# Kernel optimization log

Hardware: AMD Instinct MI355X
Metric: run time of the kernel (lower is better)

The kernel has to match this reference:

```python
import jax, jax.numpy as jnp
import numpy as np

B, S, HID = 2, 2048, 2048
H, KV, D = 16, 4, 128
G = H // KV  # kv groups
THETA = 10000.0


def setup_inputs() -> dict:
    key = jax.random.key(0)
    ks = jax.random.split(key, 6)
    x = jax.random.normal(ks[0], (B, S, HID), dtype=jnp.float32)
    wq = jax.random.normal(ks[1], (HID, H * D), dtype=jnp.float32) * 0.02
    wk = jax.random.normal(ks[2], (HID, KV * D), dtype=jnp.float32) * 0.02
    wv = jax.random.normal(ks[3], (HID, KV * D), dtype=jnp.float32) * 0.02
    wo = jax.random.normal(ks[4], (H * D, HID), dtype=jnp.float32) * 0.02
    # RoPE freqs: complex exp(i * pos * theta^{-2j/D}) -> cos/sin of shape [S, D//2]
    inv_freq = 1.0 / (THETA ** (jnp.arange(0, D, 2, dtype=jnp.float32) / D))
    ang = jnp.arange(S, dtype=jnp.float32)[:, None] * inv_freq[None, :]
    return {"x": x, "freqs_cos": jnp.cos(ang), "freqs_sin": jnp.sin(ang),
            "wq": wq, "wk": wk, "wv": wv, "wo": wo}


def _apply_rope(t, cos, sin):
    # t: [B, h, S, D]; cos/sin: [S, D//2]; complex multiply on interleaved pairs
    tr = t.reshape(*t.shape[:-1], -1, 2)
    x1, x2 = tr[..., 0], tr[..., 1]
    c = cos[None, None, :, :]
    s = sin[None, None, :, :]
    out = jnp.stack([x1 * c - x2 * s, x1 * s + x2 * c], axis=-1)
    return out.reshape(t.shape)


def reference(x, freqs_cos, freqs_sin, wq, wk, wv, wo):
    b, s, _ = x.shape
    q = (x @ wq).reshape(b, s, H, D).transpose(0, 2, 1, 3)   # [B,H,S,D]
    k = (x @ wk).reshape(b, s, KV, D).transpose(0, 2, 1, 3)  # [B,KV,S,D]
    v = (x @ wv).reshape(b, s, KV, D).transpose(0, 2, 1, 3)
    q = _apply_rope(q, freqs_cos, freqs_sin)
    k = _apply_rope(k, freqs_cos, freqs_sin)
    # GQA: group Q heads per KV head instead of expanding K/V
    qg = q.reshape(b, KV, G, s, D)
    scale = 1.0 / jnp.sqrt(jnp.asarray(D, dtype=x.dtype))
    scores = jnp.einsum('bkgqd,bksd->bkgqs', qg, k) * scale  # [B,KV,G,S,S]
    causal = jnp.tril(jnp.ones((s, s), dtype=bool))
    scores = jnp.where(causal[None, None, None], scores, jnp.finfo(scores.dtype).min)
    attn = jax.nn.softmax(scores, axis=-1)
    out = jnp.einsum('bkgqs,bksd->bkgqd', attn, v)           # [B,KV,G,S,D]
    out = out.reshape(b, H, s, D).transpose(0, 2, 1, 3).reshape(b, s, H * D)
    return (out @ wo, k, v)
```

## Files before the change

### kernel.cpp

```cpp
#include <hip/hip_runtime.h>
#include <stdint.h>

#define BB 2
#define SS 2048
#define HIDD 2048
#define HH 16
#define KVH 4
#define DD 128
#define KDIM 2048

typedef short bf16x4 __attribute__((ext_vector_type(4)));
typedef short bf16x8 __attribute__((ext_vector_type(8)));
typedef float f32x4 __attribute__((ext_vector_type(4)));
typedef float f32x16 __attribute__((ext_vector_type(16)));

__device__ __forceinline__ unsigned short f2b(float f) {
  union { float f; unsigned u; } v; v.f = f;
  unsigned r = v.u + 0x7FFFu + ((v.u >> 16) & 1u);
  return (unsigned short)(r >> 16);
}

__device__ __forceinline__ float b2f(unsigned short u) {
  union { unsigned u; float f; } v; v.u = ((unsigned)u) << 16;
  return v.f;
}

__device__ __forceinline__ unsigned cvtpk_bf16(float a, float b) {
  unsigned r;
  asm("v_cvt_pk_bf16_f32 %0, %1, %2" : "=v"(r) : "v"(a), "v"(b));
  return r;
}

__device__ __forceinline__ void gload16(const unsigned short* g, unsigned short* l) {
  __builtin_amdgcn_global_load_lds(
      (const __attribute__((address_space(1))) unsigned int*)(g),
      (__attribute__((address_space(3))) unsigned int*)(l), 16, 0, 0);
}

__device__ __forceinline__ bf16x8 ldT(const char* lds, int byteoff) {
  union { bf16x8 v; int4 q; } u;
  u.q = *reinterpret_cast<const int4*>(lds + byteoff);
  return u.v;
}

template <int N>
__device__ __forceinline__ void waitv() {
  if constexpr (N == 0) asm volatile("s_waitcnt vmcnt(0)" ::: "memory");
  else if constexpr (N == 1) asm volatile("s_waitcnt vmcnt(1)" ::: "memory");
  else if constexpr (N == 2) asm volatile("s_waitcnt vmcnt(2)" ::: "memory");
  else if constexpr (N == 3) asm volatile("s_waitcnt vmcnt(3)" ::: "memory");
  else if constexpr (N == 4) asm volatile("s_waitcnt vmcnt(4)" ::: "memory");
  else asm volatile("s_waitcnt vmcnt(6)" ::: "memory");
}

__global__ __launch_bounds__(256) void k_convert(const float* __restrict__ in,
                                                 unsigned short* __restrict__ out, int n4) {
  int i = blockIdx.x * 256 + threadIdx.x;
  int stride = gridDim.x * 256;
  for (; i < n4; i += stride) {
    float4 v = reinterpret_cast<const float4*>(in)[i];
    ushort4 o;
    o.x = f2b(v.x); o.y = f2b(v.y); o.z = f2b(v.z); o.w = f2b(v.w);
    int ci = i & 511;
    int t = ci & 7;
    int ci2 = (ci & ~7) | ((t & 3) << 1) | (t >> 2);
    reinterpret_cast<ushort4*>(out)[(i & ~511) | ci2] = o;
  }
}

__global__ __launch_bounds__(256) void k_transpose(const float* __restrict__ in,
                                                   unsigned short* __restrict__ out,
                                                   int K, int N) {
  __shared__ float tile[32][33];
  int n0 = blockIdx.x * 32, k0 = blockIdx.y * 32;
  int tx = threadIdx.x, ty = threadIdx.y;
#pragma unroll
  for (int j = 0; j < 32; j += 8)
    tile[ty + j][tx] = in[(size_t)(k0 + ty + j) * N + n0 + tx];
  __syncthreads();
  int kp = ((tx >> 2) & 3) * 8 + (tx & 3) + ((tx >> 4) << 2);
#pragma unroll
  for (int j = 0; j < 32; j += 8)
    out[(size_t)(n0 + ty + j) * K + k0 + kp] = f2b(tile[tx][ty + j]);
}

template <int EPI, int BM>
__global__ __launch_bounds__(512) void k_gemm8(
    const unsigned short* __restrict__ A, const unsigned short* __restrict__ Bt,
    float* __restrict__ outF, unsigned short* __restrict__ qws,
    unsigned short* __restrict__ kws, unsigned short* __restrict__ vTws,
    float* __restrict__ koutF, float* __restrict__ voutF,
    const float* __restrict__ cosT, const float* __restrict__ sinT) {
  constexpr int LA = BM / 128;
  constexpr int LB = 2;
  constexpr int ASTR = BM * 64;
  constexpr int BSTR = 256 * 64;
  constexpr int MF = BM / 64;
  constexpr int LSH = (BM == 256) ? 6 : 5;
  extern __shared__ __align__(16) unsigned short smem[];
  unsigned short* lAb = smem;
  unsigned short* lBb = smem + 2 * ASTR;

  const int bid = blockIdx.y * gridDim.x + blockIdx.x;
  const int nwg = gridDim.x * gridDim.y;
  const int mt = gridDim.x;
  const int swz = (bid & 7) * (nwg >> 3) + (bid >> 3);
  const int rowbase = (swz % mt) * BM;
  const int colbase = (swz / mt) * 256;

  const int tid = threadIdx.x;
  const int wv = tid >> 6, lane = tid & 63;
  const int wr = wv >> 2, wc = wv & 3;
  const int g = lane >> 4, c = lane & 15;

  const int srow8 = lane >> 3;
  const int gch = (lane & 7) ^ srow8;
  const unsigned short* aS[LA][2];
  const unsigned short* bS[2][2];
  int aOff[LA][2], bOff[2][2];
#pragma unroll
  for (int j = 0; j < LA; ++j)
#pragma unroll
    for (int h = 0; h < 2; ++h) {
      int s = wv * LA + j;
      int q = s * 8 + srow8;
      int rA = (q >> LSH) * (BM / 2) + h * (BM / 4) + (q & (BM / 4 - 1));
      aS[j][h] = A + (size_t)(rowbase + rA) * KDIM + gch * 8;
      aOff[j][h] = (h * (BM / 2) + s * 8) * 64;
    }
#pragma unroll
  for (int j = 0; j < 2; ++j)
#pragma unroll
    for (int h = 0; h < 2; ++h) {
      int s = wv * 2 + j;
      int q = s * 8 + srow8;
      int rB = (q >> 5) * 64 + h * 32 + (q & 31);
      bS[j][h] = Bt + (size_t)(colbase + rB) * KDIM + gch * 8;
      bOff[j][h] = (h * 128 + s * 8) * 64;
    }

  f32x4 acc[2 * MF][4] = {};
  bf16x8 af[MF][2], bfr[4][2];
  const int NT = KDIM / 64;

#define STAGE_A(buf, kt, h)                                               \
  _Pragma("unroll") for (int j = 0; j < LA; ++j)                          \
      gload16(aS[j][h] + (kt) * 64, lAb + (buf) * ASTR + aOff[j][h]);
#define STAGE_B(buf, kt, h)                                               \
  _Pragma("unroll") for (int j = 0; j < 2; ++j)                           \
      gload16(bS[j][h] + (kt) * 64, lBb + (buf) * BSTR + bOff[j][h]);
#define LDA(buf, mh)                                                      \
  _Pragma("unroll") for (int mm = 0; mm < MF; ++mm) {                     \
    int sr = (mh) * (BM / 2) + wr * (BM / 4) + mm * 16 + c;               \
    _Pragma("unroll") for (int kk = 0; kk < 2; ++kk) {                    \
      int slot = (kk * 4 + g) ^ (c & 7);                                  \
      af[mm][kk] = *reinterpret_cast<const bf16x8*>(                      \
          lAb + (buf) * ASTR + sr * 64 + slot * 8);                       \
    } }
#define LDB(buf, nh)                                                      \
  _Pragma("unroll") for (int nn = 0; nn < 2; ++nn) {                      \
    int sr = (nh) * 128 + wc * 32 + nn * 16 + c;                          \
    _Pragma("unroll") for (int kk = 0; kk < 2; ++kk) {                    \
      int slot = (kk * 4 + g) ^ (c & 7);                                  \
      bfr[(nh) * 2 + nn][kk] = *reinterpret_cast<const bf16x8*>(          \
          lBb + (buf) * BSTR + sr * 64 + slot * 8);                       \
    } }
#define MM(mh, nh)                                                        \
  _Pragma("unroll") for (int mm = 0; mm < MF; ++mm)                       \
  _Pragma("unroll") for (int nn = 0; nn < 2; ++nn)                        \
  _Pragma("unroll") for (int kk = 0; kk < 2; ++kk)                        \
    acc[(mh) * MF + mm][(nh) * 2 + nn] =                                  \
        __builtin_amdgcn_mfma_f32_16x16x32_bf16(                          \
            af[mm][kk], bfr[(nh) * 2 + nn][kk],                           \
            acc[(mh) * MF + mm][(nh) * 2 + nn], 0, 0, 0);
#define SCHB __builtin_amdgcn_sched_barrier(0);
#define SB __builtin_amdgcn_s_barrier();
#define LGKM asm volatile("s_waitcnt lgkmcnt(0)" ::: "memory");
#define MFMAWIN(mh, nh)                                                   \
  LGKM SCHB __builtin_amdgcn_s_setprio(1);                                \
  MM(mh, nh) __builtin_amdgcn_s_setprio(0); SCHB SB

  STAGE_A(0, 0, 0) STAGE_B(0, 0, 0) STAGE_B(0, 0, 1) STAGE_A(0, 0, 1)
  waitv<LA + LB>(); SCHB SB

  for (int kt = 0; kt < NT - 1; ++kt) {
    const int buf = kt & 1, nbuf = buf ^ 1;
    LDA(buf, 0) LDB(buf, 0)
    STAGE_A(nbuf, kt + 1, 0)
    waitv<2 * LA>(); SCHB SB
    MFMAWIN(0, 0)
    LDB(buf, 1)
    STAGE_B(nbuf, kt + 1, 0)
    waitv<LA + LB>(); SCHB SB
    MFMAWIN(0, 1)
    LDA(buf, 1)
    STAGE_B(nbuf, kt + 1, 1)
    SCHB SB
    MFMAWIN(1, 0)
    STAGE_A(nbuf, kt + 1, 1)
    waitv<LA + LB>(); SCHB SB
    MFMAWIN(1, 1)
  }
  {
    const int buf = (NT - 1) & 1;
    LDA(buf, 0) LDB(buf, 0)
    waitv<LA>(); SCHB SB
    MFMAWIN(0, 0)
    LDB(buf, 1)
    waitv<0>(); SCHB SB
    MFMAWIN(0, 1)
    LDA(buf, 1)
    SCHB SB
    MFMAWIN(1, 0)
    __builtin_amdgcn_s_setprio(1);
    MM(1, 1)
    __builtin_amdgcn_s_setprio(0);
  }

  if (EPI == 0) {
#pragma unroll
    for (int m = 0; m < 2 * MF; ++m)
#pragma unroll
      for (int n = 0; n < 4; ++n)
#pragma unroll
        for (int i = 0; i < 4; ++i) {
          int R = rowbase + wr * (BM / 2) + m * 16 + g * 4 + i;
          int Cc = colbase + wc * 64 + n * 16 + c;
          outF[(size_t)R * 2048 + Cc] = acc[m][n][i];
        }
  } else {
#pragma unroll
    for (int m = 0; m < 2 * MF; ++m) {
#pragma unroll
      for (int n = 0; n < 4; ++n) {
#pragma unroll
        for (int i = 0; i < 4; ++i) {
          float val = acc[m][n][i];
          float partner = __shfl_xor(val, 1, 64);
          int R = rowbase + wr * (BM / 2) + m * 16 + g * 4 + i;
          int Cc = colbase + wc * 64 + n * 16 + c;
          int b = R >> 11, s = R & 2047;
          int d = Cc & 127;
          int j = d >> 1;
          float cs = cosT[s * 64 + j], sn = sinT[s * 64 + j];
          float ro = ((d & 1) == 0) ? (val * cs - partner * sn)
                                    : (partner * sn + val * cs);
          if (Cc < 2048) {
            int h = Cc >> 7;
            qws[((size_t)(b * HH + h) * SS + s) * DD + d] = f2b(ro);
          } else if (Cc < 2560) {
            int kvh = (Cc - 2048) >> 7;
            size_t idx = ((size_t)(b * KVH + kvh) * SS + s) * DD + d;
            koutF[idx] = ro;
            int d16 = d & 15;
            int dp = (d & ~15) | (d16 & 3) | ((d16 & 4) << 1) | ((d16 & 8) >> 1);
            kws[((size_t)(b * KVH + kvh) * SS + s) * DD + dp] = f2b(ro);
          } else {
            int kvh = (Cc - 2560) >> 7;
            size_t idx = ((size_t)(b * KVH + kvh) * SS + s) * DD + d;
            voutF[idx] = val;
            int s16 = s & 15;
            int sp = (s & ~15) | (s16 & 3) | ((s16 & 4) << 1) | ((s16 & 8) >> 1);
            vTws[((size_t)(b * KVH + kvh) * DD + d) * SS + sp] = f2b(val);
          }
        }
      }
    }
  }
#undef STAGE_A
#undef STAGE_B
#undef LDA
#undef LDB
#undef MM
#undef SCHB
#undef SB
#undef LGKM
#undef MFMAWIN
}

__constant__ int JC[24] = {7,15,15,14,14,6,13,13,12,12,5,11,11,10,10,4,9,9,8,8,3,2,1,0};
__constant__ int JP[24] = {0,0,1, 0,1, 0,0,1, 0,1, 0,0,1, 0,1, 0,0,1, 0,1, 0,0,0,0};

__global__ __launch_bounds__(256, 2) void k_attn(const unsigned short* __restrict__ qws,
                                                 const unsigned short* __restrict__ kws,
                                                 const unsigned short* __restrict__ vT,
                                                 unsigned short* __restrict__ aows,
                                                 unsigned short* __restrict__ pO,
                                                 float* __restrict__ pml) {
  __shared__ __align__(16) char lds[2][32768];
  const int tid = threadIdx.x;
  const int lane = tid & 63;
  const int w = tid >> 6;
  const int lq = lane & 31;
  const int hi = lane >> 5;

  const int bid = blockIdx.x;
  const int j = bid >> 5;
  const int y = bid & 31;
  const int head = 4 * (y & 7) + ((y >> 3) & 3);
  const int c = JC[j];
  const int part = JP[j];
  const bool split = (c >= 8);
  const int tstart = split ? (part ? (c + 1) : 0) : 0;
  const int tend = split ? (part ? (2 * c + 2) : (c + 1)) : (2 * c + 2);

  const int b = head >> 4, h = head & 15;
  const int kv = h >> 2;
  const int q0w = c * 128 + w * 32;
  const int qg = q0w + lq;
  const float cl2 = 0.12751743f;

  const unsigned short* qp = qws + ((size_t)(b * HH + h) * SS + qg) * DD;
  bf16x8 qf[8];
#pragma unroll
  for (int ks = 0; ks < 8; ++ks) {
    union { bf16x8 v8; bf16x4 v4[2]; } u;
    const unsigned short* p = qp + ks * 16 + hi * 4;
    u.v4[0] = *reinterpret_cast<const bf16x4*>(p);
    u.v4[1] = *reinterpret_cast<const bf16x4*>(p + 8);
    qf[ks] = u.v8;
  }

  const unsigned short* kbase = kws + (size_t)(b * KVH + kv) * SS * DD;
  const unsigned short* vbase = vT + (size_t)(b * KVH + kv) * DD * SS;

  const unsigned short* kSrc[4];
  const unsigned short* vSrc[4];
  int ldsOff[4];
#pragma unroll
  for (int j2 = 0; j2 < 4; ++j2) {
    int i = w + 4 * j2;
    int ks = i >> 1, half = i & 1;
    kSrc[j2] = kbase + (size_t)(half * 32 + (lane >> 1)) * DD + ks * 16 + (lane & 1) * 8;
    int kkv = i >> 2, d0v = i & 3;
    vSrc[j2] = vbase + (size_t)(d0v * 32 + (lane >> 1)) * SS + kkv * 16 + (lane & 1) * 8;
    ldsOff[j2] = i * 1024;
  }

  auto STAGE = [&](int t, int buf) {
    char* lK = lds[buf];
    char* lV = lds[buf] + 16384;
#pragma unroll
    for (int j2 = 0; j2 < 4; ++j2) {
      gload16(kSrc[j2] + (size_t)t * 64 * DD, (unsigned short*)(lK + ldsOff[j2]));
      gload16(vSrc[j2] + (size_t)t * 64, (unsigned short*)(lV + ldsOff[j2]));
    }
  };

  f32x16 o[4] = {};
  float mrow = -1e30f, lrow = 0.f;

  STAGE(tstart, 0);
  STAGE(tstart + 1, 1);
  asm volatile("s_waitcnt vmcnt(8)" ::: "memory");
  __builtin_amdgcn_sched_barrier(0);
  __builtin_amdgcn_s_barrier();

  for (int t = tstart; t < tend; ++t) {
    const int cur = (t - tstart) & 1;

    if (t * 64 <= q0w + 31) {
      const char* lK = lds[cur];
      const char* lV = lds[cur] + 16384;
      const bool full2 = (t * 64 + 32 <= q0w + 31);

      f32x16 s0 = {}, s1 = {};
      __builtin_amdgcn_s_setprio(1);
#pragma unroll
      for (int ks = 0; ks < 8; ++ks) {
        int off = ks * 2048 + lq * 32 + hi * 16;
        s0 = __builtin_amdgcn_mfma_f32_32x32x16_bf16(ldT(lK, off), qf[ks], s0, 0, 0, 0);
      }
      if (full2) {
#pragma unroll
        for (int ks = 0; ks < 8; ++ks) {
          int off = ks * 2048 + 1024 + lq * 32 + hi * 16;
          s1 = __builtin_amdgcn_mfma_f32_32x32x16_bf16(ldT(lK, off), qf[ks], s1, 0, 0, 0);
        }
      }
      __builtin_amdgcn_s_setprio(0);

      const int kq = t * 64 + 4 * hi - qg;
      float p[32];
      float rowmax = -1e30f;
      const bool m0 = (t * 64 + 31) > q0w;
#pragma unroll
      for (int r = 0; r < 16; ++r) {
        float v = s0[r] * cl2;
        if (m0) {
          int kl = (r & 3) + 8 * (r >> 2);
          if (kq + kl > 0) v = -1e30f;
        }
        p[r] = v;
        rowmax = fmaxf(rowmax, v);
      }
      if (full2) {
        const bool m1 = (t * 64 + 63) > q0w;
#pragma unroll
        for (int r = 0; r < 16; ++r) {
          float v = s1[r] * cl2;
          if (m1) {
            int kl = 32 + (r & 3) + 8 * (r >> 2);
            if (kq + kl > 0) v = -1e30f;
          }
          p[16 + r] = v;
          rowmax = fmaxf(rowmax, v);
        }
      }
      rowmax = fmaxf(rowmax, __shfl_xor(rowmax, 32, 64));

      if (__any(rowmax > mrow + 8.f)) {
        float mnew = fmaxf(mrow, rowmax);
        float fac = exp2f(mrow - mnew);
        mrow = mnew;
        lrow *= fac;
#pragma unroll
        for (int d0 = 0; d0 < 4; ++d0)
#pragma unroll
          for (int r = 0; r < 16; ++r) o[d0][r] *= fac;
      }

      float rsum = 0.f;
#pragma unroll
      for (int e = 0; e < 16; ++e) { p[e] = exp2f(p[e] - mrow); rsum += p[e]; }
      if (full2) {
#pragma unroll
        for (int e = 16; e < 32; ++e) { p[e] = exp2f(p[e] - mrow); rsum += p[e]; }
      }
      rsum += __shfl_xor(rsum, 32, 64);
      lrow += rsum;

      bf16x8 pf[4];
#pragma unroll
      for (int s4 = 0; s4 < 2; ++s4) {
        union { bf16x8 v; unsigned u[4]; } pu;
        int base = s4 * 8;
#pragma unroll
        for (int jj = 0; jj < 4; ++jj)
          pu.u[jj] = cvtpk_bf16(p[base + 2 * jj], p[base + 2 * jj + 1]);
        pf[s4] = pu.v;
      }
      if (full2) {
#pragma unroll
        for (int s4 = 2; s4 < 4; ++s4) {
          union { bf16x8 v; unsigned u[4]; } pu;
          int base = 16 + (s4 - 2) * 8;
#pragma unroll
          for (int jj = 0; jj < 4; ++jj)
            pu.u[jj] = cvtpk_bf16(p[base + 2 * jj], p[base + 2 * jj + 1]);
          pf[s4] = pu.v;
        }
      }

      __builtin_amdgcn_s_setprio(1);
#pragma unroll
      for (int d0 = 0; d0 < 4; ++d0)
#pragma unroll
        for (int kk = 0; kk < 2; ++kk) {
          int off = (kk * 4 + d0) * 1024 + lq * 32 + hi * 16;
          o[d0] = __builtin_amdgcn_mfma_f32_32x32x16_bf16(ldT(lV, off), pf[kk], o[d0], 0, 0, 0);
        }
      if (full2) {
#pragma unroll
        for (int d0 = 0; d0 < 4; ++d0)
#pragma unroll
          for (int kk = 2; kk < 4; ++kk) {
            int off = (kk * 4 + d0) * 1024 + lq * 32 + hi * 16;
            o[d0] = __builtin_amdgcn_mfma_f32_32x32x16_bf16(ldT(lV, off), pf[kk], o[d0], 0, 0, 0);
          }
      }
      __builtin_amdgcn_s_setprio(0);
    }

    if (t + 1 < tend) {
      __builtin_amdgcn_s_barrier();
      if (t + 2 < tend) {
        STAGE(t + 2, cur);
        asm volatile("s_waitcnt vmcnt(8)" ::: "memory");
      } else {
        asm volatile("s_waitcnt vmcnt(0)" ::: "memory");
      }
      __builtin_amdgcn_sched_barrier(0);
      __builtin_amdgcn_s_barrier();
    }
  }

  if (!split) {
    float linv = 1.f / lrow;
    unsigned short* op = aows + ((size_t)(b * SS + qg)) * 2048 + h * 128;
#pragma unroll
    for (int d0 = 0; d0 < 4; ++d0)
#pragma unroll
      for (int rq = 0; rq < 4; ++rq) {
        unsigned w0 = cvtpk_bf16(o[d0][rq * 4 + 0] * linv, o[d0][rq * 4 + 1] * linv);
        unsigned w1 = cvtpk_bf16(o[d0][rq * 4 + 2] * linv, o[d0][rq * 4 + 3] * linv);
        int2 st2; st2.x = (int)w0; st2.y = (int)w1;
        int pos = 8 * ((2 * rq + hi) & 3) + 4 * (rq >> 1);
        *reinterpret_cast<int2*>(op + d0 * 32 + pos) = st2;
      }
  } else {
    int c8 = c - 8;
    int row = qg - c * 128;
    unsigned short* op = pO + ((((size_t)(head * 8 + c8) * 2 + part) * 128) + row) * 128;
#pragma unroll
    for (int d0 = 0; d0 < 4; ++d0)
#pragma unroll
      for (int rq = 0; rq < 4; ++rq) {
        unsigned w0 = cvtpk_bf16(o[d0][rq * 4 + 0], o[d0][rq * 4 + 1]);
        unsigned w1 = cvtpk_bf16(o[d0][rq * 4 + 2], o[d0][rq * 4 + 3]);
        int2 st2; st2.x = (int)w0; st2.y = (int)w1;
        *reinterpret_cast<int2*>(op + d0 * 32 + rq * 8 + hi * 4) = st2;
      }
    if (hi == 0) {
      int mlbase = (((head * 8 + c8) * 2 + part) * 2) * 128 + row;
      pml[mlbase] = mrow;
      pml[mlbase + 128] = lrow;
    }
  }
}

__global__ __launch_bounds__(256) void k_combine(const unsigned short* __restrict__ pO,
                                                 const float* __restrict__ pml,
                                                 unsigned short* __restrict__ aows) {
  int tid = blockIdx.x * 256 + threadIdx.x;
  int rg = tid >> 4;
  int d8 = tid & 15;
  int head = rg >> 10;
  int rem = rg & 1023;
  int c8 = rem >> 7;
  int row = rem & 127;
  int base2 = (head * 8 + c8) * 2;

  float m1 = pml[((base2 + 0) * 2 + 0) * 128 + row];
  float l1 = pml[((base2 + 0) * 2 + 1) * 128 + row];
  float m2 = pml[((base2 + 1) * 2 + 0) * 128 + row];
  float l2 = pml[((base2 + 1) * 2 + 1) * 128 + row];
  float m = fmaxf(m1, m2);
  float w1 = exp2f(m1 - m), w2 = exp2f(m2 - m);
  float inv = 1.f / (w1 * l1 + w2 * l2);

  const unsigned short* o1 = pO + (((size_t)(base2 + 0) * 128 + row) * 128) + d8 * 8;
  const unsigned short* o2 = pO + (((size_t)(base2 + 1) * 128 + row) * 128) + d8 * 8;
  union { int4 q; unsigned short us[8]; } ua, ub;
  ua.q = *reinterpret_cast<const int4*>(o1);
  ub.q = *reinterpret_cast<const int4*>(o2);
  float out[8];
#pragma unroll
  for (int e = 0; e < 8; ++e)
    out[e] = (w1 * b2f(ua.us[e]) + w2 * b2f(ub.us[e])) * inv;

  int b = head >> 4, h = head & 15;
  int s = (c8 + 8) * 128 + row;
  unsigned short* dst = aows + ((size_t)(b * SS + s)) * 2048 + h * 128;
  int d = d8 * 8;
  int dbase = d & ~31;
#pragma unroll
  for (int jj = 0; jj < 2; ++jj) {
    int t = ((d >> 2) + jj) & 7;
    int pos = ((t & 3) << 3) + ((t >> 2) << 2);
    unsigned wa = cvtpk_bf16(out[jj * 4 + 0], out[jj * 4 + 1]);
    unsigned wb = cvtpk_bf16(out[jj * 4 + 2], out[jj * 4 + 3]);
    int2 st2; st2.x = (int)wa; st2.y = (int)wb;
    *reinterpret_cast<int2*>(dst + dbase + pos) = st2;
  }
}

extern "C" void kernel_launch(void* const* d_in, const int* in_sizes, int n_in,
                              void* d_out, int out_size, void* d_ws, size_t ws_size,
                              hipStream_t stream) {
  (void)in_sizes; (void)n_in; (void)out_size; (void)ws_size;
  const float* x  = (const float*)d_in[0];
  const float* fc = (const float*)d_in[1];
  const float* fs = (const float*)d_in[2];
  const float* wq = (const float*)d_in[3];
  const float* wk = (const float*)d_in[4];
  const float* wv = (const float*)d_in[5];
  const float* wo = (const float*)d_in[6];
  float* out = (float*)d_out;
  float* koutF = out + (size_t)BB * SS * HIDD;
  float* voutF = koutF + (size_t)BB * KVH * SS * DD;

  unsigned short* wcatT = (unsigned short*)d_ws;
  unsigned short* woT   = wcatT + (size_t)3072 * 2048;
  unsigned short* xbf   = woT + (size_t)2048 * 2048;
  unsigned short* qws   = xbf + (size_t)4096 * 2048;
  unsigned short* kws   = qws + (size_t)BB * HH * SS * DD;
  unsigned short* vTws  = kws + (size_t)BB * KVH * SS * DD;
  unsigned short* aows  = vTws + (size_t)BB * KVH * DD * SS;

  unsigned short* pO = xbf;
  float* pml = (float*)wcatT;

  hipFuncSetAttribute((const void*)k_gemm8<1, 256>,
                      hipFuncAttributeMaxDynamicSharedMemorySize, 131072);
  hipFuncSetAttribute((const void*)k_gemm8<0, 128>,
                      hipFuncAttributeMaxDynamicSharedMemorySize, 98304);

  k_convert<<<2048, 256, 0, stream>>>(x, xbf, (int)((size_t)4096 * 2048 / 4));
  dim3 tb(32, 8);
  k_transpose<<<dim3(64, 64), tb, 0, stream>>>(wq, wcatT, 2048, 2048);
  k_transpose<<<dim3(16, 64), tb, 0, stream>>>(wk, wcatT + (size_t)2048 * 2048, 2048, 512);
  k_transpose<<<dim3(16, 64), tb, 0, stream>>>(wv, wcatT + (size_t)2560 * 2048, 2048, 512);
  k_transpose<<<dim3(64, 64), tb, 0, stream>>>(wo, woT, 2048, 2048);

  k_gemm8<1, 256><<<dim3(16, 12), 512, 131072, stream>>>(xbf, wcatT, nullptr, qws, kws,
                                                         vTws, koutF, voutF, fc, fs);
  k_attn<<<768, 256, 0, stream>>>(qws, kws, vTws, aows, pO, pml);
  k_combine<<<2048, 256, 0, stream>>>(pO, pml, aows);
  k_gemm8<0, 128><<<dim3(32, 8), 512, 98304, stream>>>(aows, woT, out, nullptr, nullptr,
                                                       nullptr, nullptr, nullptr, nullptr, nullptr);
}
```

Before: 235.8 us.

## Replace QKV projection GEMM with 128x192-tile kernel for more workgroups

Adds a dedicated QKV projection GEMM using 128x192 output tiles with a simple double-buffered direct-to-LDS pipeline, launching 512 workgroups instead of 192. The aim is better CU occupancy on a 256-CU device, where the 256x256 tiling left many CUs idle. The old fused RoPE/scatter epilogue moves into the new kernel, and the old templated GEMM is reduced to the plain output-projection path. The trade-offs are a simpler pipeline without the hand-tuned MFMA interleaving and more redundant loads of A and B tiles.

```diff
diff --git a/kernel.cpp b/kernel.cpp
--- a/kernel.cpp
+++ b/kernel.cpp
@@ -50,8 +50,10 @@
   else if constexpr (N == 2) asm volatile("s_waitcnt vmcnt(2)" ::: "memory");
   else if constexpr (N == 3) asm volatile("s_waitcnt vmcnt(3)" ::: "memory");
   else if constexpr (N == 4) asm volatile("s_waitcnt vmcnt(4)" ::: "memory");
+  else if constexpr (N == 5) asm volatile("s_waitcnt vmcnt(5)" ::: "memory");
   else asm volatile("s_waitcnt vmcnt(6)" ::: "memory");
 }
+
 
 __global__ __launch_bounds__(256) void k_convert(const float* __restrict__ in,
                                                  unsigned short* __restrict__ out, int n4) {
@@ -84,12 +86,136 @@
     out[(size_t)(n0 + ty + j) * K + k0 + kp] = f2b(tile[tx][ty + j]);
 }
 
+__global__ __launch_bounds__(512, 4) void k_gemm12(
+    const unsigned short* __restrict__ A, const unsigned short* __restrict__ Bt,
+    unsigned short* __restrict__ qws, unsigned short* __restrict__ kws,
+    unsigned short* __restrict__ vTws, float* __restrict__ koutF,
+    float* __restrict__ voutF, const float* __restrict__ cosT,
+    const float* __restrict__ sinT) {
+  __shared__ __align__(16) unsigned short lA[2][128 * 64];
+  __shared__ __align__(16) unsigned short lB[2][192 * 64];
+  const int bid = blockIdx.y * gridDim.x + blockIdx.x;
+  const int swz = (bid & 7) * 64 + (bid >> 3);
+  const int rowbase = (swz & 31) * 128;
+  const int colbase = (swz >> 5) * 192;
+  const int tid = threadIdx.x;
+  const int wv = tid >> 6, lane = tid & 63;
+  const int wr = wv >> 2, wc = wv & 3;
+  const int g = lane >> 4, c = lane & 15;
+
+  const unsigned short* aSrc[2];
+  const unsigned short* bSrc[3];
+  int aDst[2], bDst[3];
+#pragma unroll
+  for (int j = 0; j < 2; ++j) {
+    int idx = j * 512 + tid;
+    int row = idx >> 3, sl = idx & 7;
+    int gch = sl ^ (row & 7);
+    aSrc[j] = A + (size_t)(rowbase + row) * KDIM + gch * 8;
+    aDst[j] = idx * 8;
+  }
+#pragma unroll
+  for (int j = 0; j < 3; ++j) {
+    int idx = j * 512 + tid;
+    int row = idx >> 3, sl = idx & 7;
+    int gch = sl ^ (row & 7);
+    bSrc[j] = Bt + (size_t)(colbase + row) * KDIM + gch * 8;
+    bDst[j] = idx * 8;
+  }
+
+  f32x4 acc[4][3] = {};
+  const int NT = KDIM / 64;
+
+  auto STAGE = [&](int buf, int kt) {
+#pragma unroll
+    for (int j = 0; j < 2; ++j)
+      gload16(aSrc[j] + kt * 64, &lA[buf][0] + aDst[j]);
+#pragma unroll
+    for (int j = 0; j < 3; ++j)
+      gload16(bSrc[j] + kt * 64, &lB[buf][0] + bDst[j]);
+  };
+
+  STAGE(0, 0);
+  STAGE(1, 1);
+
+  for (int t = 0; t < NT; ++t) {
+    if (t + 1 < NT) { waitv<5>(); } else { waitv<0>(); }
+    __builtin_amdgcn_sched_barrier(0);
+    __builtin_amdgcn_s_barrier();
+
+    const unsigned short* la = lA[t & 1];
+    const unsigned short* lb = lB[t & 1];
+    bf16x8 bfr[3][2];
+#pragma unroll
+    for (int nn = 0; nn < 3; ++nn) {
+      int sr = wc * 48 + nn * 16 + c;
+#pragma unroll
+      for (int kk = 0; kk < 2; ++kk) {
+        int slot = (kk * 4 + g) ^ (sr & 7);
+        bfr[nn][kk] = *reinterpret_cast<const bf16x8*>(lb + sr * 64 + slot * 8);
+      }
+    }
+#pragma unroll
+    for (int mm = 0; mm < 4; ++mm) {
+      int sr = wr * 64 + mm * 16 + c;
+      int slot0 = g ^ (sr & 7);
+      int slot1 = (4 + g) ^ (sr & 7);
+      bf16x8 af0 = *reinterpret_cast<const bf16x8*>(la + sr * 64 + slot0 * 8);
+      bf16x8 af1 = *reinterpret_cast<const bf16x8*>(la + sr * 64 + slot1 * 8);
+#pragma unroll
+      for (int nn = 0; nn < 3; ++nn) {
+        acc[mm][nn] = __builtin_amdgcn_mfma_f32_16x16x32_bf16(af0, bfr[nn][0], acc[mm][nn], 0, 0, 0);
+        acc[mm][nn] = __builtin_amdgcn_mfma_f32_16x16x32_bf16(af1, bfr[nn][1], acc[mm][nn], 0, 0, 0);
+      }
+    }
+    asm volatile("s_waitcnt lgkmcnt(0)" ::: "memory");
+    __builtin_amdgcn_s_barrier();
+    if (t + 2 < NT) STAGE(t & 1, t + 2);
+  }
+
+#pragma unroll
+  for (int m = 0; m < 4; ++m) {
+#pragma unroll
+    for (int n = 0; n < 3; ++n) {
+#pragma unroll
+      for (int i = 0; i < 4; ++i) {
+        float val = acc[m][n][i];
+        float partner = __shfl_xor(val, 1, 64);
+        int R = rowbase + wr * 64 + m * 16 + g * 4 + i;
+        int Cc = colbase + wc * 48 + n * 16 + c;
+        int b = R >> 11, s = R & 2047;
+        int d = Cc & 127;
+        int j = d >> 1;
+        float cs = cosT[s * 64 + j], sn = sinT[s * 64 + j];
+        float ro = ((d & 1) == 0) ? (val * cs - partner * sn)
+                                  : (partner * sn + val * cs);
+        if (Cc < 2048) {
+          int h = Cc >> 7;
+          qws[((size_t)(b * HH + h) * SS + s) * DD + d] = f2b(ro);
+        } else if (Cc < 2560) {
+          int kvh = (Cc - 2048) >> 7;
+          size_t idx = ((size_t)(b * KVH + kvh) * SS + s) * DD + d;
+          koutF[idx] = ro;
+          int d16 = d & 15;
+          int dp = (d & ~15) | (d16 & 3) | ((d16 & 4) << 1) | ((d16 & 8) >> 1);
+          kws[((size_t)(b * KVH + kvh) * SS + s) * DD + dp] = f2b(ro);
+        } else {
+          int kvh = (Cc - 2560) >> 7;
+          size_t idx = ((size_t)(b * KVH + kvh) * SS + s) * DD + d;
+          voutF[idx] = val;
+          int s16 = s & 15;
+          int sp = (s & ~15) | (s16 & 3) | ((s16 & 4) << 1) | ((s16 & 8) >> 1);
+          vTws[((size_t)(b * KVH + kvh) * DD + d) * SS + sp] = f2b(val);
+        }
+      }
+    }
+  }
+}
+
 template <int EPI, int BM>
 __global__ __launch_bounds__(512) void k_gemm8(
     const unsigned short* __restrict__ A, const unsigned short* __restrict__ Bt,
-    float* __restrict__ outF, unsigned short* __restrict__ qws,
-    unsigned short* __restrict__ kws, unsigned short* __restrict__ vTws,
-    float* __restrict__ koutF, float* __restrict__ voutF,
+    float* __restrict__ outF,
     const float* __restrict__ cosT, const float* __restrict__ sinT) {
   constexpr int LA = BM / 128;
   constexpr int LB = 2;
@@ -217,56 +343,17 @@
     __builtin_amdgcn_s_setprio(0);
   }
 
-  if (EPI == 0) {
-#pragma unroll
-    for (int m = 0; m < 2 * MF; ++m)
-#pragma unroll
-      for (int n = 0; n < 4; ++n)
-#pragma unroll
-        for (int i = 0; i < 4; ++i) {
-          int R = rowbase + wr * (BM / 2) + m * 16 + g * 4 + i;
-          int Cc = colbase + wc * 64 + n * 16 + c;
-          outF[(size_t)R * 2048 + Cc] = acc[m][n][i];
-        }
-  } else {
-#pragma unroll
-    for (int m = 0; m < 2 * MF; ++m) {
-#pragma unroll
-      for (int n = 0; n < 4; ++n) {
-#pragma unroll
-        for (int i = 0; i < 4; ++i) {
-          float val = acc[m][n][i];
-          float partner = __shfl_xor(val, 1, 64);
-          int R = rowbase + wr * (BM / 2) + m * 16 + g * 4 + i;
-          int Cc = colbase + wc * 64 + n * 16 + c;
-          int b = R >> 11, s = R & 2047;
-          int d = Cc & 127;
-          int j = d >> 1;
-          float cs = cosT[s * 64 + j], sn = sinT[s * 64 + j];
-          float ro = ((d & 1) == 0) ? (val * cs - partner * sn)
-                                    : (partner * sn + val * cs);
-          if (Cc < 2048) {
-            int h = Cc >> 7;
-            qws[((size_t)(b * HH + h) * SS + s) * DD + d] = f2b(ro);
-          } else if (Cc < 2560) {
-            int kvh = (Cc - 2048) >> 7;
-            size_t idx = ((size_t)(b * KVH + kvh) * SS + s) * DD + d;
-            koutF[idx] = ro;
-            int d16 = d & 15;
-            int dp = (d & ~15) | (d16 & 3) | ((d16 & 4) << 1) | ((d16 & 8) >> 1);
-            kws[((size_t)(b * KVH + kvh) * SS + s) * DD + dp] = f2b(ro);
-          } else {
-            int kvh = (Cc - 2560) >> 7;
-            size_t idx = ((size_t)(b * KVH + kvh) * SS + s) * DD + d;
-            voutF[idx] = val;
-            int s16 = s & 15;
-            int sp = (s & ~15) | (s16 & 3) | ((s16 & 4) << 1) | ((s16 & 8) >> 1);
-            vTws[((size_t)(b * KVH + kvh) * DD + d) * SS + sp] = f2b(val);
-          }
-        }
-      }
-    }
-  }
+#pragma unroll
+  for (int m = 0; m < 2 * MF; ++m)
+#pragma unroll
+    for (int n = 0; n < 4; ++n)
+#pragma unroll
+      for (int i = 0; i < 4; ++i) {
+        int R = rowbase + wr * (BM / 2) + m * 16 + g * 4 + i;
+        int Cc = colbase + wc * 64 + n * 16 + c;
+        outF[(size_t)R * 2048 + Cc] = acc[m][n][i];
+      }
+  (void)cosT; (void)sinT;
 #undef STAGE_A
 #undef STAGE_B
 #undef LDA
@@ -591,8 +678,6 @@
   unsigned short* pO = xbf;
   float* pml = (float*)wcatT;
 
-  hipFuncSetAttribute((const void*)k_gemm8<1, 256>,
-                      hipFuncAttributeMaxDynamicSharedMemorySize, 131072);
   hipFuncSetAttribute((const void*)k_gemm8<0, 128>,
                       hipFuncAttributeMaxDynamicSharedMemorySize, 98304);
 
@@ -603,10 +688,9 @@
   k_transpose<<<dim3(16, 64), tb, 0, stream>>>(wv, wcatT + (size_t)2560 * 2048, 2048, 512);
   k_transpose<<<dim3(64, 64), tb, 0, stream>>>(wo, woT, 2048, 2048);
 
-  k_gemm8<1, 256><<<dim3(16, 12), 512, 131072, stream>>>(xbf, wcatT, nullptr, qws, kws,
-                                                         vTws, koutF, voutF, fc, fs);
+  k_gemm12<<<dim3(32, 16), 512, 0, stream>>>(xbf, wcatT, qws, kws, vTws,
+                                             koutF, voutF, fc, fs);
   k_attn<<<768, 256, 0, stream>>>(qws, kws, vTws, aows, pO, pml);
   k_combine<<<2048, 256, 0, stream>>>(pO, pml, aows);
-  k_gemm8<0, 128><<<dim3(32, 8), 512, 98304, stream>>>(aows, woT, out, nullptr, nullptr,
-                                                       nullptr, nullptr, nullptr, nullptr, nullptr);
-}
+  k_gemm8<0, 128><<<dim3(32, 8), 512, 98304, stream>>>(aows, woT, out, nullptr, nullptr);
+}
```

Result: faster. 216.8 us (-8.1%).
